# Kernel tuning notes

Hardware: AMD Instinct MI355X
Metric: run time of the kernel (lower is better)

The kernel has to match this reference:

```python
import jax, jax.numpy as jnp
import numpy as np
import math

B, T_FUT, T_LOOK, D, H = 8, 512, 2048, 1024, 16
HD = D // H


def setup_inputs() -> dict:
    key = jax.random.key(0)
    ks = jax.random.split(key, 12)
    xav = 1.0 / math.sqrt(D)  # approx xavier_uniform scale for square [D,D]
    return {
        "encoded_representation": jax.random.normal(ks[0], (B, T_LOOK, D), jnp.float32),
        "future_queries": jax.random.normal(ks[1], (B, T_FUT, D), jnp.float32),
        "decoder_lengths": jax.random.randint(ks[2], (B,), 1, T_FUT + 1),
        "encoder_lengths": jax.random.randint(ks[3], (B,), 1, T_LOOK + 1),
        "wq_w": jax.random.normal(ks[4], (D, D), jnp.float32) * xav,
        "wq_b": jnp.zeros((D,), jnp.float32),
        "wk_w": jax.random.normal(ks[5], (D, D), jnp.float32) * xav,
        "wk_b": jnp.zeros((D,), jnp.float32),
        "wv_w": jax.random.normal(ks[6], (D, D), jnp.float32) * xav,
        "wv_b": jnp.zeros((D,), jnp.float32),
        "wo_w": jax.random.normal(ks[7], (D, D), jnp.float32) * xav,
        "wo_b": jnp.zeros((D,), jnp.float32),
    }


def reference(encoded_representation, future_queries, decoder_lengths, encoder_lengths,
              wq_w, wq_b, wk_w, wk_b, wv_w, wv_b, wo_w, wo_b):
    # variable-length padding mask: [B, 1, T_fut, T_look]
    dec_valid = jnp.arange(T_FUT)[None, :] < decoder_lengths[:, None]   # [B, T_fut]
    enc_valid = jnp.arange(T_LOOK)[None, :] < encoder_lengths[:, None]  # [B, T_look]
    mask = dec_valid[:, None, :, None] & enc_valid[:, None, None, :]

    # torch nn.Linear: y = x @ W^T + b
    Q = (future_queries @ wq_w.T + wq_b).reshape(B, T_FUT, H, HD)
    K = (encoded_representation @ wk_w.T + wk_b).reshape(B, T_LOOK, H, HD)
    V = (encoded_representation @ wv_w.T + wv_b).reshape(B, T_LOOK, H, HD)

    scores = jnp.einsum("bqhd,bkhd->bhqk", Q, K) / math.sqrt(HD)
    # NOTE: faithful to source, which fills masked positions with -1e-09 (not -1e9)
    scores = jnp.where(mask, scores, jnp.float32(-1e-09))
    probs = jax.nn.softmax(scores, axis=-1)

    attended = jnp.einsum("bhqk,bkhd->bqhd", probs, V).reshape(B, T_FUT, D)
    return attended @ wo_w.T + wo_b
```

## Files before the change

### kernel.cpp

```cpp
#include <hip/hip_runtime.h>

typedef __attribute__((ext_vector_type(4))) float f32x4;
typedef __attribute__((ext_vector_type(8))) short s16x8;

__device__ __forceinline__ ushort f2bf(float f) {
  unsigned u = __float_as_uint(f);
  return (ushort)((u + 0x7fffu + ((u >> 16) & 1u)) >> 16);
}

__global__ __launch_bounds__(256) void cvt_bf16(const float4* __restrict__ in,
                                                ushort* __restrict__ out, int n4) {
  int stride = gridDim.x * blockDim.x;
  for (int i = blockIdx.x * blockDim.x + threadIdx.x; i < n4; i += stride) {
    float4 v = in[i];
    uint2 o;
    o.x = (unsigned)f2bf(v.x) | ((unsigned)f2bf(v.y) << 16);
    o.y = (unsigned)f2bf(v.z) | ((unsigned)f2bf(v.w) << 16);
    *(uint2*)(out + (size_t)i * 4) = o;
  }
}

__global__ __launch_bounds__(256) void cvt_bf16_w4(const float4* __restrict__ a,
                                                   const float4* __restrict__ b,
                                                   const float4* __restrict__ c,
                                                   const float4* __restrict__ d,
                                                   ushort* __restrict__ oa, ushort* __restrict__ ob,
                                                   ushort* __restrict__ oc, ushort* __restrict__ od) {
  int idx = blockIdx.x * 256 + threadIdx.x;
  int sel = idx >> 18, k = idx & 262143;
  const float4* src = sel == 0 ? a : sel == 1 ? b : sel == 2 ? c : d;
  ushort* dst = sel == 0 ? oa : sel == 1 ? ob : sel == 2 ? oc : od;
  float4 v = src[k];
  uint2 o;
  o.x = (unsigned)f2bf(v.x) | ((unsigned)f2bf(v.y) << 16);
  o.y = (unsigned)f2bf(v.z) | ((unsigned)f2bf(v.w) << 16);
  *(uint2*)(dst + (size_t)k * 4) = o;
}

__device__ __forceinline__ void gload_lds16(const void* g, void* l) {
  __builtin_amdgcn_global_load_lds((const __attribute__((address_space(1))) void*)g,
                                   (__attribute__((address_space(3))) void*)l, 16, 0, 0);
}

__device__ __forceinline__ const s16x8* ldsrd(const char* base, int row, int cb) {
  return (const s16x8*)(base + row * 128 + (cb ^ ((row & 7) << 4)));
}

__global__ __launch_bounds__(512, 1) void gemm256_kv(
    const ushort* __restrict__ A, const ushort* __restrict__ Bw,
    const float* __restrict__ biasK, const float* __restrict__ biasV,
    ushort* __restrict__ Ko, ushort* __restrict__ Vt, float* __restrict__ Tsum,
    int M, int K) {
  __shared__ char lds[131072];
  const int tid = threadIdx.x;
  const int lane = tid & 63, wid = tid >> 6;
  const int g = lane >> 4, r = lane & 15;
  const int wm = wid >> 2, wn = wid & 3;
  const int bid = blockIdx.x;
  const int n0 = (bid & 7) * 256;
  const int m0 = (bid >> 3) * 256;

  const int l8 = lane >> 3;
  const size_t rowB = (size_t)2 * K;
  const char* Ag = (const char*)A + (size_t)(m0 + wid * 8 + l8) * rowB + (((lane & 7) ^ l8) << 4);
  const char* Bg = (const char*)Bw + (size_t)(n0 + wid * 8 + l8) * rowB + (((lane & 7) ^ l8) << 4);
  const int ldst = wid * 1024;

  f32x4 acc[8][4] = {};

  auto stageA = [&](int t, int b) {
    char* d = lds + b * 32768 + ldst;
    const char* s = Ag + (size_t)t * 128;
#pragma unroll
    for (int c = 0; c < 4; ++c) gload_lds16(s + (size_t)c * 64 * rowB, d + c * 8192);
  };
  auto stageB = [&](int t, int b) {
    char* d = lds + 65536 + b * 32768 + ldst;
    const char* s = Bg + (size_t)t * 128;
#pragma unroll
    for (int c = 0; c < 4; ++c) gload_lds16(s + (size_t)c * 64 * rowB, d + c * 8192);
  };

  stageA(0, 0);
  stageB(0, 0);
  asm volatile("s_waitcnt vmcnt(0)" ::: "memory");
  __builtin_amdgcn_s_barrier();

  const int NT = K >> 6;

#define GPHASE(I0, EXTRA)                                                                  \
  {                                                                                        \
    s16x8 aq[2][2];                                                                        \
    _Pragma("unroll") for (int i = 0; i < 2; ++i)                                          \
        _Pragma("unroll") for (int kk = 0; kk < 2; ++kk)                                   \
            aq[i][kk] = *ldsrd(Ab, wm * 128 + (I0 + i) * 16 + r, kk * 64 + g * 16);        \
    EXTRA;                                                                                 \
    __builtin_amdgcn_s_barrier();                                                          \
    asm volatile("s_waitcnt lgkmcnt(0)" ::: "memory");                                     \
    __builtin_amdgcn_sched_barrier(0);                                                     \
    __builtin_amdgcn_s_setprio(1);                                                         \
    _Pragma("unroll") for (int i = 0; i < 2; ++i)                                          \
        _Pragma("unroll") for (int ni = 0; ni < 4; ++ni)                                   \
            _Pragma("unroll") for (int kk = 0; kk < 2; ++kk)                               \
                acc[I0 + i][ni] = __builtin_amdgcn_mfma_f32_16x16x32_bf16(                 \
                    aq[i][kk], bf[ni][kk], acc[I0 + i][ni], 0, 0, 0);                      \
    __builtin_amdgcn_s_setprio(0);                                                         \
  }

  for (int t = 0; t < NT; ++t) {
    const int cb_ = t & 1, nb_ = cb_ ^ 1;
    const char* Ab = lds + cb_ * 32768;
    const char* Bb = lds + 65536 + cb_ * 32768;
    const bool more = (t + 1 < NT);
    s16x8 bf[4][2];
#pragma unroll
    for (int ni = 0; ni < 4; ++ni)
#pragma unroll
      for (int kk = 0; kk < 2; ++kk)
        bf[ni][kk] = *ldsrd(Bb, wn * 64 + ni * 16 + r, kk * 64 + g * 16);

    GPHASE(0, if (more) stageA(t + 1, nb_));
    __builtin_amdgcn_s_barrier();
    GPHASE(2, if (more) stageB(t + 1, nb_));
    __builtin_amdgcn_s_barrier();
    GPHASE(4, );
    __builtin_amdgcn_s_barrier();
    GPHASE(6, );
    if (more) asm volatile("s_waitcnt vmcnt(0)" ::: "memory");
    __builtin_amdgcn_s_barrier();
  }
#undef GPHASE

  if (n0 < 1024) {
#pragma unroll
    for (int ni = 0; ni < 4; ++ni) {
      const int n = n0 + wn * 64 + ni * 16 + r;
      const float bv = biasK[n];
#pragma unroll
      for (int i = 0; i < 8; ++i) {
        const int mb = m0 + wm * 128 + i * 16 + g * 4;
#pragma unroll
        for (int j = 0; j < 4; ++j)
          Ko[(size_t)(mb + j) * 1024 + n] = f2bf(acc[i][ni][j] + bv);
      }
    }
  } else {
#pragma unroll
    for (int ni = 0; ni < 4; ++ni) {
      const int nv = n0 - 1024 + wn * 64 + ni * 16 + r;
      const float bv = biasV[nv];
#pragma unroll
      for (int i = 0; i < 8; ++i) {
        const int mb = m0 + wm * 128 + i * 16 + g * 4;
        const int bbi = mb >> 11, tt = mb & 2047;
        uint2 val;
        val.x = (unsigned)f2bf(acc[i][ni][0] + bv) | ((unsigned)f2bf(acc[i][ni][1] + bv) << 16);
        val.y = (unsigned)f2bf(acc[i][ni][2] + bv) | ((unsigned)f2bf(acc[i][ni][3] + bv) << 16);
        *(uint2*)(Vt + ((size_t)bbi * 1024 + nv) * 2048 + tt) = val;
      }
#pragma unroll
      for (int hf = 0; hf < 2; ++hf) {
        float s = 0.0f;
#pragma unroll
        for (int i = hf * 4; i < hf * 4 + 4; ++i)
#pragma unroll
          for (int j = 0; j < 4; ++j) s += acc[i][ni][j];
        s += __shfl_xor(s, 16);
        s += __shfl_xor(s, 32);
        if (g == 0) {
          const int gt = (m0 + wm * 128 + hf * 64) >> 6;
          const int bbi = gt >> 5, tl = gt & 31;
          Tsum[((size_t)(bbi * 16 + (nv >> 6)) * 33 + tl) * 64 + (nv & 63)] = s + 64.0f * bv;
        }
      }
    }
  }
}

template <int EPI>
__global__ __launch_bounds__(256) void gemm_bt(const ushort* __restrict__ A,
                                               const ushort* __restrict__ B,
                                               const float* __restrict__ bias,
                                               void* __restrict__ Cout, float oscale,
                                               int M, int N, int K) {
  __shared__ ushort As[128 * 32];
  __shared__ ushort Bs[128 * 32];
  const int tid = threadIdx.x;
  const int lane = tid & 63, w = tid >> 6;
  const int g = lane >> 4, r = lane & 15;
  const int m0 = blockIdx.x * 128, n0 = blockIdx.y * 128;
  const int wm = (w >> 1) * 64, wn = (w & 1) * 64;

  const int srow = tid >> 2;
  const int scb = (tid & 3) * 16;
  const char* Ag = (const char*)(A + (size_t)(m0 + srow) * K) + scb;
  const char* Bg = (const char*)(B + (size_t)(n0 + srow) * K) + scb;
  char* AsB = (char*)As + (tid & 192) * 16;
  char* BsB = (char*)Bs + (tid & 192) * 16;
  const size_t rowskip = (size_t)64 * K * sizeof(ushort);

  f32x4 acc[4][4] = {};

  for (int k0 = 0; k0 < K; k0 += 32) {
    gload_lds16(Ag + (size_t)k0 * 2, AsB);
    gload_lds16(Ag + rowskip + (size_t)k0 * 2, AsB + 4096);
    gload_lds16(Bg + (size_t)k0 * 2, BsB);
    gload_lds16(Bg + rowskip + (size_t)k0 * 2, BsB + 4096);
    __syncthreads();
    s16x8 af[4], bf[4];
#pragma unroll
    for (int i = 0; i < 4; ++i) af[i] = *(const s16x8*)&As[(wm + i * 16 + r) * 32 + g * 8];
#pragma unroll
    for (int i = 0; i < 4; ++i) bf[i] = *(const s16x8*)&Bs[(wn + i * 16 + r) * 32 + g * 8];
#pragma unroll
    for (int mi = 0; mi < 4; ++mi)
#pragma unroll
      for (int ni = 0; ni < 4; ++ni)
        acc[mi][ni] =
            __builtin_amdgcn_mfma_f32_16x16x32_bf16(af[mi], bf[ni], acc[mi][ni], 0, 0, 0);
    __syncthreads();
  }

  if constexpr (EPI == 0) {
    ushort* C = (ushort*)Cout;
#pragma unroll
    for (int ni = 0; ni < 4; ++ni) {
      const int n = n0 + wn + ni * 16 + r;
      const float bv = bias[n];
#pragma unroll
      for (int mi = 0; mi < 4; ++mi) {
        const int mb = m0 + wm + mi * 16 + g * 4;
#pragma unroll
        for (int j = 0; j < 4; ++j)
          C[(size_t)(mb + j) * N + n] = f2bf((acc[mi][ni][j] + bv) * oscale);
      }
    }
  } else {
    float* C = (float*)Cout;
#pragma unroll
    for (int ni = 0; ni < 4; ++ni) {
      const int n = n0 + wn + ni * 16 + r;
      const float bv = bias[n];
#pragma unroll
      for (int mi = 0; mi < 4; ++mi) {
        const int mb = m0 + wm + mi * 16 + g * 4;
#pragma unroll
        for (int j = 0; j < 4; ++j)
          C[(size_t)(mb + j) * N + n] = acc[mi][ni][j] + bv;
      }
    }
  }
}

__global__ __launch_bounds__(64) void vsuffix(float* __restrict__ T) {
  const int bh = blockIdx.x;
  const int d = threadIdx.x;
  float* p = T + (size_t)bh * 33 * 64 + d;
  float run = 0.0f;
  p[32 * 64] = 0.0f;
  for (int t = 31; t >= 0; --t) {
    run += p[t * 64];
    p[t * 64] = run;
  }
}

__device__ __forceinline__ ushort* swz(ushort* base, int row, int colb) {
  return (ushort*)((char*)base + row * 128 + (colb ^ ((row & 7) << 4)));
}

__global__ __launch_bounds__(256) void attn_fwd(
    const ushort* __restrict__ Q, const ushort* __restrict__ Km,
    const ushort* __restrict__ Vt, const float* __restrict__ Vsuf,
    const int* __restrict__ dlen, const int* __restrict__ elen,
    ushort* __restrict__ Oatt) {
  const int tid = threadIdx.x;
  const int lane = tid & 63, w = tid >> 6;
  const int g = lane >> 4, r = lane & 15;
  const int qt = blockIdx.x, b = blockIdx.y, h = blockIdx.z;
  const int dl = dlen[b], el = elen[b];
  const float* VS = Vsuf + (size_t)(b * 16 + h) * 33 * 64;

  if (qt * 64 >= dl) {
    const int qrow = qt * 64 + w * 16 + g * 4;
#pragma unroll
    for (int dt = 0; dt < 4; ++dt) {
      const ushort hv = f2bf(VS[dt * 16 + r] * (1.0f / 2048.0f));
#pragma unroll
      for (int j = 0; j < 4; ++j)
        Oatt[(size_t)(b * 512 + qrow + j) * 1024 + h * 64 + dt * 16 + r] = hv;
    }
    return;
  }

  __shared__ ushort Ks[64 * 64];
  __shared__ ushort Vs[64 * 64];
  __shared__ ushort Ps[4 * 16 * 64];
  ushort* PsW = Ps + w * 16 * 64;
  const int qbase = qt * 64 + w * 16;

  s16x8 qf[2];
  {
    const ushort* qp = Q + (size_t)(b * 512 + qbase + r) * 1024 + h * 64 + g * 8;
    qf[0] = *(const s16x8*)qp;
    qf[1] = *(const s16x8*)(qp + 32);
  }

  f32x4 o[4] = {};
  float lrow[4] = {0.0f, 0.0f, 0.0f, 0.0f};
  bool qok[4];
#pragma unroll
  for (int j = 0; j < 4; ++j) qok[j] = (qbase + g * 4 + j) < dl;

  const int sr = tid >> 3;
  const int sc8 = (tid & 7) * 8;
  const int scb = sc8 * 2;
  const ushort* Kg = Km + (size_t)(b * 2048 + sr) * 1024 + h * 64 + sc8;
  const ushort* Vg = Vt + ((size_t)b * 1024 + h * 64 + sr) * 2048 + sc8;

  const int t_last = (el - 1) >> 6;

  s16x8 pk0, pk1, pv0, pv1;
  {
    pk0 = *(const s16x8*)(Kg);
    pk1 = *(const s16x8*)(Kg + (size_t)32 * 1024);
    pv0 = *(const s16x8*)(Vg);
    pv1 = *(const s16x8*)(Vg + (size_t)32 * 2048);
  }

  for (int t = 0; t <= t_last; ++t) {
    *(s16x8*)swz(Ks, sr, scb) = pk0;
    *(s16x8*)swz(Ks, sr + 32, scb) = pk1;
    *(s16x8*)swz(Vs, sr, scb) = pv0;
    *(s16x8*)swz(Vs, sr + 32, scb) = pv1;
    __syncthreads();

    if (t < t_last) {
      const int kv0 = (t + 1) * 64;
      pk0 = *(const s16x8*)(Kg + (size_t)kv0 * 1024);
      pk1 = *(const s16x8*)(Kg + (size_t)(kv0 + 32) * 1024);
      pv0 = *(const s16x8*)(Vg + kv0);
      pv1 = *(const s16x8*)(Vg + (size_t)32 * 2048 + kv0);
    }

    const int kv0 = t * 64;
    float p[4][4];
#pragma unroll
    for (int nt = 0; nt < 4; ++nt) {
      f32x4 s = {};
      s16x8 kf0 = *(const s16x8*)swz(Ks, nt * 16 + r, g * 16);
      s16x8 kf1 = *(const s16x8*)swz(Ks, nt * 16 + r, 64 + g * 16);
      s = __builtin_amdgcn_mfma_f32_16x16x32_bf16(qf[0], kf0, s, 0, 0, 0);
      s = __builtin_amdgcn_mfma_f32_16x16x32_bf16(qf[1], kf1, s, 0, 0, 0);
      const bool kok = (kv0 + nt * 16 + r) < el;
#pragma unroll
      for (int j = 0; j < 4; ++j) {
        const float pe = __builtin_amdgcn_exp2f(s[j]);
        p[nt][j] = (kok && qok[j]) ? pe : 1.0f;
      }
    }
#pragma unroll
    for (int nt = 0; nt < 4; ++nt)
#pragma unroll
      for (int j = 0; j < 4; ++j) lrow[j] += p[nt][j];

#pragma unroll
    for (int nt = 0; nt < 4; ++nt) {
#pragma unroll
      for (int jp = 0; jp < 4; jp += 2) {
        unsigned pk;
        asm("v_cvt_pk_bf16_f32 %0, %1, %2" : "=v"(pk) : "v"(p[nt][jp]), "v"(p[nt][jp + 1]));
        *swz(PsW, g * 4 + jp, (nt * 16 + r) * 2) = (ushort)pk;
        *swz(PsW, g * 4 + jp + 1, (nt * 16 + r) * 2) = (ushort)(pk >> 16);
      }
    }

#pragma unroll
    for (int kc = 0; kc < 2; ++kc) {
      s16x8 pf = *(const s16x8*)swz(PsW, r, kc * 64 + g * 16);
#pragma unroll
      for (int dt = 0; dt < 4; ++dt) {
        s16x8 vf = *(const s16x8*)swz(Vs, dt * 16 + r, kc * 64 + g * 16);
        o[dt] = __builtin_amdgcn_mfma_f32_16x16x32_bf16(pf, vf, o[dt], 0, 0, 0);
      }
    }
    __syncthreads();
  }

  const float tailcnt = (float)(2048 - (t_last + 1) * 64);
  const float* VT = VS + (t_last + 1) * 64;
#pragma unroll
  for (int dt = 0; dt < 4; ++dt) {
    const float tv = VT[dt * 16 + r];
#pragma unroll
    for (int j = 0; j < 4; ++j) o[dt][j] += tv;
  }

  float inv[4];
#pragma unroll
  for (int j = 0; j < 4; ++j) {
    float s = lrow[j];
    s += __shfl_xor(s, 1);
    s += __shfl_xor(s, 2);
    s += __shfl_xor(s, 4);
    s += __shfl_xor(s, 8);
    inv[j] = 1.0f / (s + tailcnt);
  }
#pragma unroll
  for (int dt = 0; dt < 4; ++dt)
#pragma unroll
    for (int j = 0; j < 4; ++j)
      Oatt[(size_t)(b * 512 + qbase + g * 4 + j) * 1024 + h * 64 + dt * 16 + r] =
          f2bf(o[dt][j] * inv[j]);
}

extern "C" void kernel_launch(void* const* d_in, const int* in_sizes, int n_in,
                              void* d_out, int out_size, void* d_ws, size_t ws_size,
                              hipStream_t stream) {
  const float* enc  = (const float*)d_in[0];
  const float* fq   = (const float*)d_in[1];
  const int* dlen   = (const int*)d_in[2];
  const int* elen   = (const int*)d_in[3];
  const float* wq_w = (const float*)d_in[4];
  const float* wq_b = (const float*)d_in[5];
  const float* wk_w = (const float*)d_in[6];
  const float* wk_b = (const float*)d_in[7];
  const float* wv_w = (const float*)d_in[8];
  const float* wv_b = (const float*)d_in[9];
  const float* wo_w = (const float*)d_in[10];
  const float* wo_b = (const float*)d_in[11];

  char* ws = (char*)d_ws;
  ushort* enc16 = (ushort*)(ws + 0);
  ushort* fq16  = (ushort*)(ws + 33554432);
  float*  Vsuf  = (float*)(ws + 33554432);
  ushort* wq16  = (ushort*)(ws + 41943040);
  ushort* wk16  = (ushort*)(ws + 44040192);
  ushort* wv16  = (ushort*)(ws + 46137344);
  ushort* wo16  = (ushort*)(ws + 48234496);
  ushort* Qw    = (ushort*)(ws + 50331648);
  ushort* Kw    = (ushort*)(ws + 58720256);
  ushort* Vtw   = (ushort*)(ws + 92274688);
  ushort* attw  = (ushort*)(ws + 125829120);

  cvt_bf16<<<2048, 256, 0, stream>>>((const float4*)enc, enc16, 16384 * 1024 / 4);
  cvt_bf16<<<1024, 256, 0, stream>>>((const float4*)fq, fq16, 4096 * 1024 / 4);
  cvt_bf16_w4<<<4096, 256, 0, stream>>>((const float4*)wq_w, (const float4*)wk_w,
                                        (const float4*)wv_w, (const float4*)wo_w,
                                        wq16, wk16, wv16, wo16);

  const float qscale = 0.125f * 1.44269504088896340736f;
  gemm_bt<0><<<dim3(32, 8), 256, 0, stream>>>(fq16, wq16, wq_b, Qw, qscale, 4096, 1024, 1024);

  gemm256_kv<<<512, 512, 0, stream>>>(enc16, wk16, wk_b, wv_b, Kw, Vtw, Vsuf, 16384, 1024);
  vsuffix<<<128, 64, 0, stream>>>(Vsuf);

  attn_fwd<<<dim3(8, 8, 16), 256, 0, stream>>>(Qw, Kw, Vtw, Vsuf, dlen, elen, attw);

  gemm_bt<2><<<dim3(32, 8), 256, 0, stream>>>(attw, wo16, wo_b, d_out, 1.0f, 4096, 1024, 1024);
}
```

Measured before the change: 216.5 us.

## Deepen KV GEMM prefetch to two tiles ahead with partial vmcnt waits

Restructures the 256x256 KV-projection GEMM so global-to-LDS loads are issued two K-tiles ahead, split into per-quarter chunks spread across the four compute phases, and waits only with vmcnt(7) instead of draining all loads each iteration. The load mapping is flattened to one 16-byte chunk per thread per quarter, and each warp's A rows are interleaved (32-row stride) instead of contiguous. This changes which rows each warp owns, so the V column-sum epilogue now combines partials from the two warp rows through LDS with extra barriers. It aims to hide global memory latency behind MFMA work, at the cost of more complex wait accounting.

```diff
diff --git a/kernel.cpp b/kernel.cpp
--- a/kernel.cpp
+++ b/kernel.cpp
@@ -60,58 +60,56 @@
   const int n0 = (bid & 7) * 256;
   const int m0 = (bid >> 3) * 256;
 
-  const int l8 = lane >> 3;
   const size_t rowB = (size_t)2 * K;
-  const char* Ag = (const char*)A + (size_t)(m0 + wid * 8 + l8) * rowB + (((lane & 7) ^ l8) << 4);
-  const char* Bg = (const char*)Bw + (size_t)(n0 + wid * 8 + l8) * rowB + (((lane & 7) ^ l8) << 4);
-  const int ldst = wid * 1024;
+  const char* Ag0 = (const char*)A + (size_t)(m0 + (tid >> 3)) * rowB +
+                    ((size_t)((tid & 7) ^ ((tid >> 3) & 7)) << 4);
+  const char* Bg0 = (const char*)Bw + (size_t)(n0 + (tid >> 3)) * rowB +
+                    ((size_t)((tid & 7) ^ ((tid >> 3) & 7)) << 4);
 
   f32x4 acc[8][4] = {};
 
-  auto stageA = [&](int t, int b) {
-    char* d = lds + b * 32768 + ldst;
-    const char* s = Ag + (size_t)t * 128;
-#pragma unroll
-    for (int c = 0; c < 4; ++c) gload_lds16(s + (size_t)c * 64 * rowB, d + c * 8192);
+  auto sA = [&](int t, int q) {
+    gload_lds16(Ag0 + (size_t)q * 64 * rowB + (size_t)t * 128,
+                lds + (t & 1) * 32768 + q * 8192 + tid * 16);
   };
-  auto stageB = [&](int t, int b) {
-    char* d = lds + 65536 + b * 32768 + ldst;
-    const char* s = Bg + (size_t)t * 128;
-#pragma unroll
-    for (int c = 0; c < 4; ++c) gload_lds16(s + (size_t)c * 64 * rowB, d + c * 8192);
+  auto sB = [&](int t, int q) {
+    gload_lds16(Bg0 + (size_t)q * 64 * rowB + (size_t)t * 128,
+                lds + 65536 + (t & 1) * 32768 + q * 8192 + tid * 16);
   };
 
-  stageA(0, 0);
-  stageB(0, 0);
-  asm volatile("s_waitcnt vmcnt(0)" ::: "memory");
+  const int NT = K >> 6;
+
+  sA(0, 0); sA(0, 1); sA(0, 2); sA(0, 3);
+  sB(0, 0); sB(0, 1); sB(0, 2); sB(0, 3);
+  sA(1, 0); sB(1, 0); sB(1, 1);
+  sA(1, 1); sB(1, 2); sB(1, 3);
+  sA(1, 2);
+  asm volatile("s_waitcnt vmcnt(7)" ::: "memory");
   __builtin_amdgcn_s_barrier();
-
-  const int NT = K >> 6;
 
 #define GPHASE(I0, EXTRA)                                                                  \
   {                                                                                        \
     s16x8 aq[2][2];                                                                        \
-    _Pragma("unroll") for (int i = 0; i < 2; ++i)                                          \
+    _Pragma("unroll") for (int ii = 0; ii < 2; ++ii)                                       \
         _Pragma("unroll") for (int kk = 0; kk < 2; ++kk)                                   \
-            aq[i][kk] = *ldsrd(Ab, wm * 128 + (I0 + i) * 16 + r, kk * 64 + g * 16);        \
+            aq[ii][kk] = *ldsrd(Ab, (I0 + ii) * 32 + wm * 16 + r, kk * 64 + g * 16);       \
     EXTRA;                                                                                 \
     __builtin_amdgcn_s_barrier();                                                          \
     asm volatile("s_waitcnt lgkmcnt(0)" ::: "memory");                                     \
     __builtin_amdgcn_sched_barrier(0);                                                     \
     __builtin_amdgcn_s_setprio(1);                                                         \
-    _Pragma("unroll") for (int i = 0; i < 2; ++i)                                          \
+    _Pragma("unroll") for (int ii = 0; ii < 2; ++ii)                                       \
         _Pragma("unroll") for (int ni = 0; ni < 4; ++ni)                                   \
             _Pragma("unroll") for (int kk = 0; kk < 2; ++kk)                               \
-                acc[I0 + i][ni] = __builtin_amdgcn_mfma_f32_16x16x32_bf16(                 \
-                    aq[i][kk], bf[ni][kk], acc[I0 + i][ni], 0, 0, 0);                      \
+                acc[I0 + ii][ni] = __builtin_amdgcn_mfma_f32_16x16x32_bf16(                \
+                    aq[ii][kk], bf[ni][kk], acc[I0 + ii][ni], 0, 0, 0);                    \
     __builtin_amdgcn_s_setprio(0);                                                         \
   }
 
   for (int t = 0; t < NT; ++t) {
-    const int cb_ = t & 1, nb_ = cb_ ^ 1;
-    const char* Ab = lds + cb_ * 32768;
-    const char* Bb = lds + 65536 + cb_ * 32768;
-    const bool more = (t + 1 < NT);
+    const char* Ab = lds + (t & 1) * 32768;
+    const char* Bb = lds + 65536 + (t & 1) * 32768;
+    const bool m1 = (t + 1 < NT), m2 = (t + 2 < NT);
     s16x8 bf[4][2];
 #pragma unroll
     for (int ni = 0; ni < 4; ++ni)
@@ -119,14 +117,17 @@
       for (int kk = 0; kk < 2; ++kk)
         bf[ni][kk] = *ldsrd(Bb, wn * 64 + ni * 16 + r, kk * 64 + g * 16);
 
-    GPHASE(0, if (more) stageA(t + 1, nb_));
+    GPHASE(0, if (m1) sA(t + 1, 3));
     __builtin_amdgcn_s_barrier();
-    GPHASE(2, if (more) stageB(t + 1, nb_));
+    GPHASE(2, if (m2) { sA(t + 2, 0); sB(t + 2, 0); sB(t + 2, 1); });
     __builtin_amdgcn_s_barrier();
-    GPHASE(4, );
+    GPHASE(4, if (m2) { sA(t + 2, 1); sB(t + 2, 2); sB(t + 2, 3); });
     __builtin_amdgcn_s_barrier();
-    GPHASE(6, );
-    if (more) asm volatile("s_waitcnt vmcnt(0)" ::: "memory");
+    GPHASE(6, if (m2) sA(t + 2, 2));
+    if (t < NT - 2)
+      asm volatile("s_waitcnt vmcnt(7)" ::: "memory");
+    else
+      asm volatile("s_waitcnt vmcnt(0)" ::: "memory");
     __builtin_amdgcn_s_barrier();
   }
 #undef GPHASE
@@ -138,39 +139,61 @@
       const float bv = biasK[n];
 #pragma unroll
       for (int i = 0; i < 8; ++i) {
-        const int mb = m0 + wm * 128 + i * 16 + g * 4;
+        const int mb = m0 + i * 32 + wm * 16 + g * 4;
 #pragma unroll
         for (int j = 0; j < 4; ++j)
           Ko[(size_t)(mb + j) * 1024 + n] = f2bf(acc[i][ni][j] + bv);
       }
     }
   } else {
+    float* Lts = (float*)lds;
 #pragma unroll
     for (int ni = 0; ni < 4; ++ni) {
       const int nv = n0 - 1024 + wn * 64 + ni * 16 + r;
       const float bv = biasV[nv];
 #pragma unroll
       for (int i = 0; i < 8; ++i) {
-        const int mb = m0 + wm * 128 + i * 16 + g * 4;
+        const int mb = m0 + i * 32 + wm * 16 + g * 4;
         const int bbi = mb >> 11, tt = mb & 2047;
         uint2 val;
         val.x = (unsigned)f2bf(acc[i][ni][0] + bv) | ((unsigned)f2bf(acc[i][ni][1] + bv) << 16);
         val.y = (unsigned)f2bf(acc[i][ni][2] + bv) | ((unsigned)f2bf(acc[i][ni][3] + bv) << 16);
         *(uint2*)(Vt + ((size_t)bbi * 1024 + nv) * 2048 + tt) = val;
       }
-#pragma unroll
-      for (int hf = 0; hf < 2; ++hf) {
+    }
+    float part[4][4];
+#pragma unroll
+    for (int ni = 0; ni < 4; ++ni)
+#pragma unroll
+      for (int q = 0; q < 4; ++q) {
         float s = 0.0f;
 #pragma unroll
-        for (int i = hf * 4; i < hf * 4 + 4; ++i)
-#pragma unroll
-          for (int j = 0; j < 4; ++j) s += acc[i][ni][j];
+        for (int ii = 0; ii < 2; ++ii)
+#pragma unroll
+          for (int j = 0; j < 4; ++j) s += acc[2 * q + ii][ni][j];
         s += __shfl_xor(s, 16);
         s += __shfl_xor(s, 32);
-        if (g == 0) {
-          const int gt = (m0 + wm * 128 + hf * 64) >> 6;
+        part[ni][q] = s;
+      }
+    __syncthreads();
+    if (wm == 0 && g == 0) {
+#pragma unroll
+      for (int ni = 0; ni < 4; ++ni)
+#pragma unroll
+        for (int q = 0; q < 4; ++q) Lts[q * 256 + wn * 64 + ni * 16 + r] = part[ni][q];
+    }
+    __syncthreads();
+    if (wm == 1 && g == 0) {
+#pragma unroll
+      for (int ni = 0; ni < 4; ++ni) {
+        const int nv = n0 - 1024 + wn * 64 + ni * 16 + r;
+        const float bv = biasV[nv];
+#pragma unroll
+        for (int q = 0; q < 4; ++q) {
+          const int gt = (m0 + q * 64) >> 6;
           const int bbi = gt >> 5, tl = gt & 31;
-          Tsum[((size_t)(bbi * 16 + (nv >> 6)) * 33 + tl) * 64 + (nv & 63)] = s + 64.0f * bv;
+          Tsum[((size_t)(bbi * 16 + (nv >> 6)) * 33 + tl) * 64 + (nv & 63)] =
+              part[ni][q] + Lts[q * 256 + wn * 64 + ni * 16 + r] + 64.0f * bv;
         }
       }
     }
```

Measured after the change: 220.5 us. Within noise of the previous version (+1.9%).
